# Performance work log

Hardware: AMD Instinct MI355X
Metric: run time of the kernel (lower is better)

Reference implementation:

```python
import jax, jax.numpy as jnp
import numpy as np
from jax import lax

IDC = 8          # in_dim_caps
ROUTINGS = 3
BN_EPS = 1e-5


def squash(s, axis=-1):
    mag_sq = jnp.sum(s * s, axis=axis, keepdims=True)
    mag = jnp.sqrt(mag_sq)
    return mag_sq / (1.0 + mag_sq) * (s / (mag + 1e-8))


def setup_inputs() -> dict:
    key = jax.random.key(0)
    ks = jax.random.split(key, 8)
    B, P, S = 64, 512, 8
    O, OD, Z = 32, 16, 64
    I = S * S * (P // IDC)  # 4096 input capsules
    return {
        "x": jax.random.normal(ks[0], (B, P, S, S), jnp.float32),
        "conv_w": 0.02 * jax.random.normal(ks[1], (P, P, 3, 3), jnp.float32),
        "bn_gamma": jnp.ones((P,), jnp.float32),
        "bn_beta": jnp.zeros((P,), jnp.float32),
        "bn_mean": jnp.zeros((P,), jnp.float32),
        "bn_var": jnp.ones((P,), jnp.float32),
        "caps_w": 0.01 * jax.random.normal(ks[2], (O, I, OD, IDC), jnp.float32),
        "fcm_w1": 0.02 * jax.random.normal(ks[3], (OD, 1024), jnp.float32),
        "fcm_b1": jnp.zeros((1024,), jnp.float32),
        "fcm_w2": 0.02 * jax.random.normal(ks[4], (1024, Z), jnp.float32),
        "fcm_b2": jnp.zeros((Z,), jnp.float32),
        "fcv_w": 0.02 * jax.random.normal(ks[5], (OD, Z), jnp.float32),
        "fcv_b": jnp.zeros((Z,), jnp.float32),
    }


def reference(x, conv_w, bn_gamma, bn_beta, bn_mean, bn_var, caps_w,
              fcm_w1, fcm_b1, fcm_w2, fcm_b2, fcv_w, fcv_b):
    # conv_pose: Conv3x3 (no bias) -> BatchNorm (eval, running stats) -> ReLU
    y = lax.conv_general_dilated(x, conv_w, (1, 1), 'SAME',
                                 dimension_numbers=('NCHW', 'OIHW', 'NCHW'))
    inv = bn_gamma / jnp.sqrt(bn_var + BN_EPS)
    y = (y - bn_mean[None, :, None, None]) * inv[None, :, None, None] + bn_beta[None, :, None, None]
    y = jax.nn.relu(y)

    B, P, S, _ = y.shape
    # [B, P//IDC, IDC, S, S] -> [B, P//IDC, S, S, IDC] -> [B, I, IDC]
    pose = y.reshape(B, P // IDC, IDC, S, S).transpose(0, 1, 3, 4, 2).reshape(B, -1, IDC)
    pose = squash(pose)

    # x_hat[b,o,i,d] = sum_k W[o,i,d,k] * pose[b,i,k]
    x_hat = jnp.einsum('oidk,bik->boid', caps_w, pose)
    x_hat_d = lax.stop_gradient(x_hat)

    b = jnp.zeros(x_hat.shape[:3], x_hat.dtype)  # [B, O, I]
    out = None
    for i in range(ROUTINGS):
        c = jax.nn.softmax(b, axis=1)  # softmax over output capsules
        if i == ROUTINGS - 1:
            out = squash(jnp.einsum('boi,boid->bod', c, x_hat))
        else:
            v = squash(jnp.einsum('boi,boid->bod', c, x_hat_d))
            b = b + jnp.einsum('bod,boid->boi', v, x_hat_d)

    # VAE head (eval mode: z = z_mu)
    h = jax.nn.relu(out @ fcm_w1 + fcm_b1)
    z_mu = h @ fcm_w2 + fcm_b2
    z_var = jax.nn.softplus(out @ fcv_w + fcv_b) + 1e-8
    z = z_mu
    return (z, z_mu, z_var)
```

## Files before the change

kernel.cpp:

```cpp
#include <hip/hip_runtime.h>
#include <cstdint>
#include <cstddef>

#define B 64
#define PCH 512
#define O_CAPS 32
#define OD 16
#define IDC 8
#define I_CAPS 4096
#define KDIM 4608

typedef __attribute__((ext_vector_type(8))) short bf16x8;
typedef __attribute__((ext_vector_type(4))) float f32x4;
typedef __attribute__((ext_vector_type(8))) unsigned short u16x8;
typedef _Float16 h2 __attribute__((ext_vector_type(2)));
typedef _Float16 f16x8v __attribute__((ext_vector_type(8)));

#define OFF_PH 0
#define SZ_PH (B * I_CAPS * IDC / 2)
#define OFF_PART (OFF_PH + SZ_PH)
#define SZ_PART ((size_t)256 * 4 * 16 * 512)
#define OFF_AIM OFF_PART
#define OFF_PV OFF_PART
#define OFF_CH (OFF_PART + 1048576)
#define OFF_SPILL (OFF_PART + SZ_PART)
#define OFF_VBUF (OFF_SPILL + 1048576)
#define SZ_V (B * O_CAPS * OD)
#define OFF_VBUF2 (OFF_VBUF + SZ_V)
#define OFF_OUTC (OFF_VBUF2 + SZ_V)
#define OFF_WB (OFF_OUTC + SZ_V)
#define OFF_BIAS (OFF_WB + (PCH * KDIM) / 2)
#define OFF_WRH (OFF_BIAS + 512)
#define SZ_WRH ((size_t)O_CAPS * I_CAPS * OD * IDC / 2)

__device__ inline unsigned short f2bf(float f) {
  union { float f; unsigned int u; } v; v.f = f;
  unsigned int r = v.u + 0x7fff + ((v.u >> 16) & 1);
  return (unsigned short)(r >> 16);
}

union HU { u16x8 v; f16x8v f; _Float16 h[8]; h2 p[4]; };

__device__ inline unsigned short f2h(float f) {
  union { _Float16 h; unsigned short u; } c;
  c.h = (_Float16)f;
  return c.u;
}

__device__ inline float h2f(unsigned short u) {
  union { unsigned short u; _Float16 h; } c;
  c.u = u;
  return (float)c.h;
}

__global__ __launch_bounds__(256) void cast_f16x8(
    const float* __restrict__ src, unsigned short* __restrict__ dst) {
  const size_t t = (size_t)blockIdx.x * 256 + threadIdx.x;
  const float4* s = (const float4*)src + t * 2;
  const float4 a = s[0], b = s[1];
  HU u;
  u.h[0] = (_Float16)a.x; u.h[1] = (_Float16)a.y;
  u.h[2] = (_Float16)a.z; u.h[3] = (_Float16)a.w;
  u.h[4] = (_Float16)b.x; u.h[5] = (_Float16)b.y;
  u.h[6] = (_Float16)b.z; u.h[7] = (_Float16)b.w;
  ((u16x8*)dst)[t] = u.v;
}

__global__ __launch_bounds__(256) void prep_wb(
    const float* __restrict__ cw, const float* __restrict__ gamma,
    const float* __restrict__ beta, const float* __restrict__ mean,
    const float* __restrict__ var, unsigned short* __restrict__ wb,
    float* __restrict__ bias) {
  const int n = blockIdx.x;
  const float inv = gamma[n] * rsqrtf(var[n] + 1e-5f);
  if (threadIdx.x == 0) bias[n] = beta[n] - mean[n] * inv;
  for (int k = threadIdx.x; k < KDIM; k += 256)
    wb[(size_t)n * KDIM + k] = f2bf(cw[(size_t)n * KDIM + k] * inv);
}

__global__ __launch_bounds__(256) void prep_aim(
    const float* __restrict__ x, unsigned short* __restrict__ aim) {
  __shared__ float lxp[32 * 100];
  const int b = blockIdx.x;
  const int ci0 = blockIdx.y * 32;
  const int tid = threadIdx.x;
  for (int t = tid; t < 3200; t += 256) lxp[t] = 0.f;
  __syncthreads();
  for (int t = tid; t < 2048; t += 256) {
    const int ci = t >> 6, px = t & 63;
    lxp[ci * 100 + 11 + (px >> 3) * 10 + (px & 7)] =
        x[((size_t)b * PCH + ci0 + ci) * 64 + px];
  }
  __syncthreads();
  for (int t = tid; t < 4608; t += 256) {
    const int px = t / 72;
    const int kk = (t - px * 72) * 4;
    unsigned short v[4];
#pragma unroll
    for (int j = 0; j < 4; ++j) {
      const int k = kk + j;
      const int ci = k / 9;
      const int tap = k - ci * 9;
      const int kh = tap / 3, kw = tap - kh * 3;
      v[j] = f2bf(lxp[ci * 100 + ((px >> 3) + kh) * 10 + (px & 7) + kw]);
    }
    ushort4* dst =
        (ushort4*)(aim + (size_t)(b * 64 + px) * KDIM + ci0 * 9 + kk);
    *dst = make_ushort4(v[0], v[1], v[2], v[3]);
  }
}

__global__ __launch_bounds__(256) void conv_gemm(
    const unsigned short* __restrict__ aim, const unsigned short* __restrict__ wb,
    const float* __restrict__ bias, unsigned short* __restrict__ pose_h) {
  __shared__ unsigned short lA[64 * 64];
  __shared__ unsigned short lB[64 * 64];
  const int tid = threadIdx.x;
  const int lane = tid & 63, wv = tid >> 6;
  const int wm = wv & 1, wn = wv >> 1;
  const int m0 = blockIdx.x * 64;
  const int n0 = blockIdx.y * 64;
  const int rsub = lane >> 3, seg = lane & 7;

  f32x4 acc[2][2];
#pragma unroll
  for (int a = 0; a < 2; ++a)
#pragma unroll
    for (int c = 0; c < 2; ++c) acc[a][c] = (f32x4){0.f, 0.f, 0.f, 0.f};

  for (int k0 = 0; k0 < KDIM; k0 += 64) {
    __syncthreads();
#pragma unroll
    for (int it = 0; it < 2; ++it) {
      const int r = it * 32 + wv * 8 + rsub;
      const int c = seg ^ (r & 7);
      const unsigned short* ga = aim + (size_t)(m0 + r) * KDIM + k0 + c * 8;
      __builtin_amdgcn_global_load_lds(
          (const __attribute__((address_space(1))) void*)ga,
          (__attribute__((address_space(3))) void*)(lA + (it * 32 + wv * 8) * 64),
          16, 0, 0);
      const unsigned short* gb = wb + (size_t)(n0 + r) * KDIM + k0 + c * 8;
      __builtin_amdgcn_global_load_lds(
          (const __attribute__((address_space(1))) void*)gb,
          (__attribute__((address_space(3))) void*)(lB + (it * 32 + wv * 8) * 64),
          16, 0, 0);
    }
    __syncthreads();
#pragma unroll
    for (int kc = 0; kc < 2; ++kc) {
      const int g = kc * 4 + (lane >> 4);
      const int ml = wm * 32 + (lane & 15);
      const int nl = wn * 32 + (lane & 15);
      const int sa = (g ^ (ml & 7)) * 8;
      const int sb = (g ^ (nl & 7)) * 8;
      const bf16x8 a0 = *(const bf16x8*)(lA + (ml + 0) * 64 + sa);
      const bf16x8 a1 = *(const bf16x8*)(lA + (ml + 16) * 64 + sa);
      const bf16x8 b0 = *(const bf16x8*)(lB + (nl + 0) * 64 + sb);
      const bf16x8 b1 = *(const bf16x8*)(lB + (nl + 16) * 64 + sb);
      acc[0][0] = __builtin_amdgcn_mfma_f32_16x16x32_bf16(a0, b0, acc[0][0], 0, 0, 0);
      acc[0][1] = __builtin_amdgcn_mfma_f32_16x16x32_bf16(a0, b1, acc[0][1], 0, 0, 0);
      acc[1][0] = __builtin_amdgcn_mfma_f32_16x16x32_bf16(a1, b0, acc[1][0], 0, 0, 0);
      acc[1][1] = __builtin_amdgcn_mfma_f32_16x16x32_bf16(a1, b1, acc[1][1], 0, 0, 0);
    }
  }

  const int bq = blockIdx.x;
  float bsv[2];
#pragma unroll
  for (int ni = 0; ni < 2; ++ni)
    bsv[ni] = bias[n0 + wn * 32 + ni * 16 + (lane & 15)];
#pragma unroll
  for (int mi = 0; mi < 2; ++mi) {
#pragma unroll
    for (int ni = 0; ni < 2; ++ni) {
      const int n = n0 + wn * 32 + ni * 16 + (lane & 15);
#pragma unroll
      for (int reg = 0; reg < 4; ++reg) {
        float v = fmaxf(acc[mi][ni][reg] + bsv[ni], 0.f);
        float s2 = v * v;
        s2 += __shfl_xor(s2, 1, 64);
        s2 += __shfl_xor(s2, 2, 64);
        s2 += __shfl_xor(s2, 4, 64);
        const float sc = s2 / (1.f + s2) / (sqrtf(s2) + 1e-8f);
        const int px = wm * 32 + mi * 16 + (lane >> 4) * 4 + reg;
        pose_h[((size_t)bq * I_CAPS + (n >> 3) * 64 + px) * IDC + (n & 7)] =
            f2h(v * sc);
      }
    }
  }
}

__global__ __launch_bounds__(256) void caps_v0(
    const unsigned short* __restrict__ pose_h,
    const unsigned short* __restrict__ wrh, float* __restrict__ pv) {
  __shared__ unsigned short lA[64 * 64];
  __shared__ unsigned short lB[64 * 64];
  const int tid = threadIdx.x;
  const int lane = tid & 63, wv = tid >> 6;
  const int wm = wv & 1, wn = wv >> 1;
  const int o0 = blockIdx.x * 4;
  const int ks = blockIdx.y;
  const int rsub = lane >> 3, seg = lane & 7;

  f32x4 acc[2][2];
#pragma unroll
  for (int a = 0; a < 2; ++a)
#pragma unroll
    for (int c = 0; c < 2; ++c) acc[a][c] = (f32x4){0.f, 0.f, 0.f, 0.f};

  for (int kt = 0; kt < 16; ++kt) {
    const int k0 = ks * 1024 + kt * 64;
    const int i0 = k0 >> 3;
    __syncthreads();
#pragma unroll
    for (int it = 0; it < 2; ++it) {
      const int r = it * 32 + wv * 8 + rsub;
      const int c = seg ^ (r & 7);
      const unsigned short* ga = pose_h + (size_t)r * 32768 + k0 + c * 8;
      __builtin_amdgcn_global_load_lds(
          (const __attribute__((address_space(1))) void*)ga,
          (__attribute__((address_space(3))) void*)(lA + (it * 32 + wv * 8) * 64),
          16, 0, 0);
    }
#pragma unroll
    for (int h = 0; h < 2; ++h) {
      const int idx = h * 256 + tid;
      const int d = idx & 15;
      const int il = (idx >> 4) & 7;
      const int ol = idx >> 7;
      const u16x8 v = *(const u16x8*)(wrh + (size_t)(o0 + ol) * 524288 +
                                      (size_t)(i0 + il) * 128 + d * 8);
      const int np = ol * 16 + d;
      *(u16x8*)(lB + np * 64 + (il ^ (np & 7)) * 8) = v;
    }
    __syncthreads();
#pragma unroll
    for (int kc = 0; kc < 2; ++kc) {
      const int g = kc * 4 + (lane >> 4);
      const int ml = wm * 32 + (lane & 15);
      const int nl = wn * 32 + (lane & 15);
      const int sa = (g ^ (ml & 7)) * 8;
      const int sb = (g ^ (nl & 7)) * 8;
      const f16x8v a0 = *(const f16x8v*)(lA + (ml + 0) * 64 + sa);
      const f16x8v a1 = *(const f16x8v*)(lA + (ml + 16) * 64 + sa);
      const f16x8v b0 = *(const f16x8v*)(lB + (nl + 0) * 64 + sb);
      const f16x8v b1 = *(const f16x8v*)(lB + (nl + 16) * 64 + sb);
      acc[0][0] = __builtin_amdgcn_mfma_f32_16x16x32_f16(a0, b0, acc[0][0], 0, 0, 0);
      acc[0][1] = __builtin_amdgcn_mfma_f32_16x16x32_f16(a0, b1, acc[0][1], 0, 0, 0);
      acc[1][0] = __builtin_amdgcn_mfma_f32_16x16x32_f16(a1, b0, acc[1][0], 0, 0, 0);
      acc[1][1] = __builtin_amdgcn_mfma_f32_16x16x32_f16(a1, b1, acc[1][1], 0, 0, 0);
    }
  }
#pragma unroll
  for (int mi = 0; mi < 2; ++mi) {
#pragma unroll
    for (int ni = 0; ni < 2; ++ni) {
      const int n = blockIdx.x * 64 + wn * 32 + ni * 16 + (lane & 15);
#pragma unroll
      for (int reg = 0; reg < 4; ++reg) {
        const int m = wm * 32 + mi * 16 + (lane >> 4) * 4 + reg;
        pv[(size_t)(ks * 64 + m) * 512 + n] = acc[mi][ni][reg];
      }
    }
  }
}

__global__ __launch_bounds__(256) void out_gemm(
    const unsigned short* __restrict__ pose_h,
    const unsigned short* __restrict__ wrh,
    const unsigned short* __restrict__ ch, float* __restrict__ pv) {
  __shared__ unsigned short lA[64 * 64];
  __shared__ unsigned short lB[64 * 64];
  __shared__ unsigned short clds[4 * 64 * 8];
  const int tid = threadIdx.x;
  const int lane = tid & 63, wv = tid >> 6;
  const int wm = wv & 1, wn = wv >> 1;
  const int o0 = blockIdx.x * 4;
  const int ks = blockIdx.y;
  const int rsub = lane >> 3, seg = lane & 7;
  const _Float16* chl = (const _Float16*)clds;

  f32x4 acc[2][2];
#pragma unroll
  for (int a = 0; a < 2; ++a)
#pragma unroll
    for (int c = 0; c < 2; ++c) acc[a][c] = (f32x4){0.f, 0.f, 0.f, 0.f};

  for (int kt = 0; kt < 16; ++kt) {
    const int k0 = ks * 1024 + kt * 64;
    const int i0 = k0 >> 3;
    __syncthreads();
#pragma unroll
    for (int it = 0; it < 2; ++it) {
      const int r = it * 32 + wv * 8 + rsub;
      const int c = seg ^ (r & 7);
      const unsigned short* ga = pose_h + (size_t)r * 32768 + k0 + c * 8;
      __builtin_amdgcn_global_load_lds(
          (const __attribute__((address_space(1))) void*)ga,
          (__attribute__((address_space(3))) void*)(lA + (it * 32 + wv * 8) * 64),
          16, 0, 0);
    }
#pragma unroll
    for (int h = 0; h < 2; ++h) {
      const int idx = h * 256 + tid;
      const int d = idx & 15;
      const int il = (idx >> 4) & 7;
      const int ol = idx >> 7;
      const u16x8 v = *(const u16x8*)(wrh + (size_t)(o0 + ol) * 524288 +
                                      (size_t)(i0 + il) * 128 + d * 8);
      const int np = ol * 16 + d;
      *(u16x8*)(lB + np * 64 + (il ^ (np & 7)) * 8) = v;
    }
    {
      const int o_l = tid >> 6, cb = tid & 63;
      const uint4 cv = *(const uint4*)(ch + (size_t)(o0 + o_l) * (B * I_CAPS) +
                                       (size_t)cb * I_CAPS + i0);
      *(uint4*)&clds[(o_l * 64 + cb) * 8] = cv;
    }
    __syncthreads();
#pragma unroll
    for (int kc = 0; kc < 2; ++kc) {
      const int g = kc * 4 + (lane >> 4);
      const int ml = wm * 32 + (lane & 15);
      const int nl = wn * 32 + (lane & 15);
      const int sa = (g ^ (ml & 7)) * 8;
      const int sb = (g ^ (nl & 7)) * 8;
      const f16x8v a0 = *(const f16x8v*)(lA + (ml + 0) * 64 + sa);
      const f16x8v a1 = *(const f16x8v*)(lA + (ml + 16) * 64 + sa);
      const f16x8v b0 = *(const f16x8v*)(lB + (nl + 0) * 64 + sb);
      const f16x8v b1 = *(const f16x8v*)(lB + (nl + 16) * 64 + sb);
      const int ol0 = wn * 2, ol1 = wn * 2 + 1;
      const _Float16 c00 = chl[(ol0 * 64 + ml) * 8 + g];
      const _Float16 c01 = chl[(ol1 * 64 + ml) * 8 + g];
      const _Float16 c10 = chl[(ol0 * 64 + ml + 16) * 8 + g];
      const _Float16 c11 = chl[(ol1 * 64 + ml + 16) * 8 + g];
      acc[0][0] = __builtin_amdgcn_mfma_f32_16x16x32_f16(a0 * c00, b0, acc[0][0], 0, 0, 0);
      acc[0][1] = __builtin_amdgcn_mfma_f32_16x16x32_f16(a0 * c01, b1, acc[0][1], 0, 0, 0);
      acc[1][0] = __builtin_amdgcn_mfma_f32_16x16x32_f16(a1 * c10, b0, acc[1][0], 0, 0, 0);
      acc[1][1] = __builtin_amdgcn_mfma_f32_16x16x32_f16(a1 * c11, b1, acc[1][1], 0, 0, 0);
    }
  }
#pragma unroll
  for (int mi = 0; mi < 2; ++mi) {
#pragma unroll
    for (int ni = 0; ni < 2; ++ni) {
      const int n = blockIdx.x * 64 + wn * 32 + ni * 16 + (lane & 15);
#pragma unroll
      for (int reg = 0; reg < 4; ++reg) {
        const int m = wm * 32 + mi * 16 + (lane >> 4) * 4 + reg;
        pv[(size_t)(ks * 64 + m) * 512 + n] = acc[mi][ni][reg];
      }
    }
  }
}

__global__ __launch_bounds__(256) void logits_softmax(
    const unsigned short* __restrict__ pose_h,
    const unsigned short* __restrict__ wrh,
    const float* __restrict__ vb, unsigned short* __restrict__ ch) {
  __shared__ unsigned short ppose[16 * 132];
  __shared__ float lgl[32 * 272];
  const int tid = threadIdx.x;
  const int lane = tid & 63, wv = tid >> 6;
  const int i0 = blockIdx.x * 16;
  const int b0 = blockIdx.y * 16;
  const _Float16* wh = (const _Float16*)wrh;

  {
    const int b = tid >> 4, i = tid & 15;
    const ushort4* src =
        (const ushort4*)(pose_h + ((size_t)(b0 + b) * I_CAPS + (i0 + i)) * IDC);
    const ushort4 p0 = src[0], p1 = src[1];
    *(ushort4*)&ppose[b * 132 + i * 8] = p0;
    *(ushort4*)&ppose[b * 132 + i * 8 + 4] = p1;
  }
  __syncthreads();

  const int m = lane & 15;
  const int g = lane >> 4;
  const int a_isub = m >> 3, a_kk = m & 7;
  const int c_isub = g >> 1, c_kk0 = (g & 1) * 4;

  for (int o = 0; o < 32; ++o) {
    HU bu;
    bu.v = (u16x8){0, 0, 0, 0, 0, 0, 0, 0};
    if (g < 2) {
      const float4* vp =
          (const float4*)(vb + ((size_t)(b0 + m) * O_CAPS + o) * OD + g * 8);
      const float4 v0 = vp[0], v1 = vp[1];
      bu.h[0] = (_Float16)v0.x; bu.h[1] = (_Float16)v0.y;
      bu.h[2] = (_Float16)v0.z; bu.h[3] = (_Float16)v0.w;
      bu.h[4] = (_Float16)v1.x; bu.h[5] = (_Float16)v1.y;
      bu.h[6] = (_Float16)v1.z; bu.h[7] = (_Float16)v1.w;
    }
#pragma unroll
    for (int q = 0; q < 2; ++q) {
      const int ip = wv * 2 + q;
      HU au;
      au.v = (u16x8){0, 0, 0, 0, 0, 0, 0, 0};
      if (g < 2) {
        const int ii = i0 + ip * 2 + a_isub;
        const size_t base =
            (((size_t)o * I_CAPS + ii) * OD + g * 8) * IDC + a_kk;
#pragma unroll
        for (int j = 0; j < 8; ++j) au.h[j] = wh[base + (size_t)j * IDC];
      }
      const f32x4 C = __builtin_amdgcn_mfma_f32_16x16x32_f16(
          au.f, bu.f, (f32x4){0.f, 0.f, 0.f, 0.f}, 0, 0, 0);
      const ushort4 pk =
          *(const ushort4*)&ppose[m * 132 + (ip * 2 + c_isub) * 8 + c_kk0];
      float tmp = C[0] * h2f(pk.x) + C[1] * h2f(pk.y) + C[2] * h2f(pk.z) +
                  C[3] * h2f(pk.w);
      tmp += __shfl_xor(tmp, 16, 64);
      if ((lane & 16) == 0) {
        const int iw = ip * 2 + (lane >> 5);
        lgl[o * 272 + iw * 17 + m] = tmp;
      }
    }
  }
  __syncthreads();

  {
    const int i = tid & 15, b = tid >> 4;
    float e[32];
    float sm = 0.f;
#pragma unroll
    for (int o = 0; o < 32; ++o) {
      e[o] = __expf(lgl[o * 272 + i * 17 + b]);
      sm += e[o];
    }
    const float r = 1.f / sm;
#pragma unroll
    for (int o = 0; o < 32; ++o)
      ch[(size_t)o * ((size_t)B * I_CAPS) + (size_t)(b0 + b) * I_CAPS +
         (i0 + i)] = f2h(e[o] * r);
  }
}

template <int SCALE32, int ADDV>
__global__ __launch_bounds__(256) void reduce_pv(
    const float* __restrict__ pv, const float* __restrict__ vprev,
    float* __restrict__ dst) {
  const int t = blockIdx.x * 256 + threadIdx.x;
  const int b = t >> 9;
  const int r = t & 511;
  float s = 0.f;
#pragma unroll 8
  for (int ks = 0; ks < 32; ++ks)
    s += pv[(size_t)(ks * 64 + b) * 512 + r];
  if (SCALE32) s *= (1.0f / 32.0f);
  float sq = s * s;
  sq += __shfl_xor(sq, 1, 64);
  sq += __shfl_xor(sq, 2, 64);
  sq += __shfl_xor(sq, 4, 64);
  sq += __shfl_xor(sq, 8, 64);
  const float sc = sq / (1.f + sq) / (sqrtf(sq) + 1e-8f);
  float val = s * sc;
  if (ADDV) val += vprev[t];
  dst[t] = val;
}

__global__ __launch_bounds__(1024) void vae_head(
    const float* __restrict__ outc, const float* __restrict__ w1,
    const float* __restrict__ b1, const float* __restrict__ w2,
    const float* __restrict__ b2, const float* __restrict__ wv,
    const float* __restrict__ bv, float* __restrict__ dout) {
  __shared__ float lo[4][16];
  __shared__ float lh[4][1024];
  __shared__ float red[16][4][64];
  const int n0 = blockIdx.x * 4;
  const int tid = threadIdx.x;
  if (tid < 64) lo[tid >> 4][tid & 15] = outc[(size_t)n0 * 16 + tid];
  __syncthreads();

  {
    const float bb = b1[tid];
    float h0 = bb, h1 = bb, h2v = bb, h3 = bb;
#pragma unroll
    for (int k = 0; k < 16; ++k) {
      const float w = w1[(size_t)k * 1024 + tid];
      h0 += lo[0][k] * w;
      h1 += lo[1][k] * w;
      h2v += lo[2][k] * w;
      h3 += lo[3][k] * w;
    }
    lh[0][tid] = fmaxf(h0, 0.f);
    lh[1][tid] = fmaxf(h1, 0.f);
    lh[2][tid] = fmaxf(h2v, 0.f);
    lh[3][tid] = fmaxf(h3, 0.f);
  }
  __syncthreads();

  const int m = tid & 63, sl = tid >> 6;
  {
    float a0 = 0.f, a1 = 0.f, a2 = 0.f, a3 = 0.f;
    const int j0 = sl * 64;
#pragma unroll 4
    for (int jj = 0; jj < 64; ++jj) {
      const int j = j0 + jj;
      const float w = w2[(size_t)j * 64 + m];
      a0 += lh[0][j] * w;
      a1 += lh[1][j] * w;
      a2 += lh[2][j] * w;
      a3 += lh[3][j] * w;
    }
    red[sl][0][m] = a0;
    red[sl][1][m] = a1;
    red[sl][2][m] = a2;
    red[sl][3][m] = a3;
  }
  __syncthreads();

  if (tid < 256) {
    const int r = tid >> 6;
    float z = b2[m];
#pragma unroll
    for (int s = 0; s < 16; ++s) z += red[s][r][m];
    const int n = n0 + r;
    dout[n * 64 + m] = z;
    dout[131072 + n * 64 + m] = z;
    float sv = bv[m];
#pragma unroll
    for (int k = 0; k < 16; ++k) sv += lo[r][k] * wv[(size_t)k * 64 + m];
    const float sp =
        (sv > 0.f) ? (sv + log1pf(__expf(-sv))) : log1pf(__expf(sv));
    dout[262144 + n * 64 + m] = sp + 1e-8f;
  }
}

extern "C" void kernel_launch(void* const* d_in, const int* in_sizes, int n_in,
                              void* d_out, int out_size, void* d_ws,
                              size_t ws_size, hipStream_t stream) {
  const float* x = (const float*)d_in[0];
  const float* conv_w = (const float*)d_in[1];
  const float* bn_gamma = (const float*)d_in[2];
  const float* bn_beta = (const float*)d_in[3];
  const float* bn_mean = (const float*)d_in[4];
  const float* bn_var = (const float*)d_in[5];
  const float* caps_w = (const float*)d_in[6];
  const float* fcm_w1 = (const float*)d_in[7];
  const float* fcm_b1 = (const float*)d_in[8];
  const float* fcm_w2 = (const float*)d_in[9];
  const float* fcm_b2 = (const float*)d_in[10];
  const float* fcv_w = (const float*)d_in[11];
  const float* fcv_b = (const float*)d_in[12];
  float* out = (float*)d_out;
  float* ws = (float*)d_ws;

  unsigned short* pose_h = (unsigned short*)(ws + OFF_PH);
  float* pv = ws + OFF_PV;
  unsigned short* ch = (unsigned short*)(ws + OFF_CH);
  float* vbuf = ws + OFF_VBUF;
  float* vbuf2 = ws + OFF_VBUF2;
  float* outc = ws + OFF_OUTC;
  unsigned short* wbq = (unsigned short*)(ws + OFF_WB);
  float* bias = ws + OFF_BIAS;
  unsigned short* wrh = (unsigned short*)(ws + OFF_WRH);
  unsigned short* aim = (unsigned short*)(ws + OFF_AIM);

  cast_f16x8<<<8192, 256, 0, stream>>>(caps_w, wrh);
  prep_wb<<<512, 256, 0, stream>>>(conv_w, bn_gamma, bn_beta, bn_mean, bn_var,
                                   wbq, bias);
  prep_aim<<<dim3(64, 16), 256, 0, stream>>>(x, aim);
  conv_gemm<<<dim3(64, 8), 256, 0, stream>>>(aim, wbq, bias, pose_h);

  caps_v0<<<dim3(8, 32), 256, 0, stream>>>(pose_h, wrh, pv);
  reduce_pv<1, 0><<<128, 256, 0, stream>>>(pv, nullptr, vbuf);

  logits_softmax<<<dim3(256, 4), 256, 0, stream>>>(pose_h, wrh, vbuf, ch);
  out_gemm<<<dim3(8, 32), 256, 0, stream>>>(pose_h, wrh, ch, pv);
  reduce_pv<0, 1><<<128, 256, 0, stream>>>(pv, vbuf, vbuf2);

  logits_softmax<<<dim3(256, 4), 256, 0, stream>>>(pose_h, wrh, vbuf2, ch);
  out_gemm<<<dim3(8, 32), 256, 0, stream>>>(pose_h, wrh, ch, pv);
  reduce_pv<0, 0><<<128, 256, 0, stream>>>(pv, nullptr, outc);

  vae_head<<<512, 1024, 0, stream>>>(outc, fcm_w1, fcm_b1, fcm_w2, fcm_b2,
                                     fcv_w, fcv_b, out);
}
```

Before: 380.8 us.

## Stage weight tiles through LDS and keep routing logits in registers

The logits_softmax kernel used to gather the fp16 capsule weights with strided scalar global loads inside the MFMA loop. It now loads them in chunks of 8 output capsules using coalesced 16-byte loads, transposes them into an LDS tile, and reads MFMA operands from LDS as vectors. The logits are also kept in a per-thread register array instead of a large shared buffer, which removes that LDS staging and the final sync. The costs are extra barriers per chunk, higher register pressure from the 32-element array, and a changed write pattern for ch.

```diff
diff --git a/kernel.cpp b/kernel.cpp
--- a/kernel.cpp
+++ b/kernel.cpp
@@ -9,6 +9,7 @@
 #define IDC 8
 #define I_CAPS 4096
 #define KDIM 4608
+#define OCH 8
 
 typedef __attribute__((ext_vector_type(8))) short bf16x8;
 typedef __attribute__((ext_vector_type(4))) float f32x4;
@@ -359,12 +360,11 @@
     const unsigned short* __restrict__ wrh,
     const float* __restrict__ vb, unsigned short* __restrict__ ch) {
   __shared__ unsigned short ppose[16 * 132];
-  __shared__ float lgl[32 * 272];
+  __shared__ unsigned short wlds[OCH * 16 * 8 * 16];
   const int tid = threadIdx.x;
   const int lane = tid & 63, wv = tid >> 6;
   const int i0 = blockIdx.x * 16;
   const int b0 = blockIdx.y * 16;
-  const _Float16* wh = (const _Float16*)wrh;
 
   {
     const int b = tid >> 4, i = tid & 15;
@@ -374,67 +374,86 @@
     *(ushort4*)&ppose[b * 132 + i * 8] = p0;
     *(ushort4*)&ppose[b * 132 + i * 8 + 4] = p1;
   }
-  __syncthreads();
 
   const int m = lane & 15;
   const int g = lane >> 4;
-  const int a_isub = m >> 3, a_kk = m & 7;
-  const int c_isub = g >> 1, c_kk0 = (g & 1) * 4;
-
+  const int a_kk = m & 7;
+  const int gq = g & 1;
+  const int c_isub = g >> 1;
+  const int c_kk0 = (g & 1) * 4;
+
+  const int s_o2 = tid >> 7, s_i = (tid >> 3) & 15, s_dp = tid & 7;
+  unsigned int* wl32 = (unsigned int*)wlds;
+
+  float e[32];
+
+#pragma unroll
+  for (int og = 0; og < 32; og += OCH) {
+    __syncthreads();
+#pragma unroll
+    for (int pp = 0; pp < OCH / 2; ++pp) {
+      const int ol = pp * 2 + s_o2;
+      const int o = og + ol;
+      const unsigned short* gsrc =
+          wrh + ((size_t)o * I_CAPS + (i0 + s_i)) * 128 + s_dp * 16;
+      const u16x8 wa = *(const u16x8*)gsrc;
+      const u16x8 wc = *(const u16x8*)(gsrc + 8);
+      const int rbase = (ol * 16 + s_i) * 8;
+#pragma unroll
+      for (int k = 0; k < 8; ++k) {
+        wl32[(rbase + k) * 8 + s_dp] =
+            (unsigned int)(unsigned short)wa[k] |
+            ((unsigned int)(unsigned short)wc[k] << 16);
+      }
+    }
+    __syncthreads();
+#pragma unroll
+    for (int ol = 0; ol < OCH; ++ol) {
+      const int o = og + ol;
+      HU bu;
+      bu.v = (u16x8){0, 0, 0, 0, 0, 0, 0, 0};
+      if (g < 2) {
+        const float4* vp =
+            (const float4*)(vb + ((size_t)(b0 + m) * O_CAPS + o) * OD + g * 8);
+        const float4 v0 = vp[0], v1 = vp[1];
+        bu.h[0] = (_Float16)v0.x; bu.h[1] = (_Float16)v0.y;
+        bu.h[2] = (_Float16)v0.z; bu.h[3] = (_Float16)v0.w;
+        bu.h[4] = (_Float16)v1.x; bu.h[5] = (_Float16)v1.y;
+        bu.h[6] = (_Float16)v1.z; bu.h[7] = (_Float16)v1.w;
+      }
+#pragma unroll
+      for (int q = 0; q < 2; ++q) {
+        const int ip = wv * 2 + q;
+        HU au;
+        au.v = (u16x8){0, 0, 0, 0, 0, 0, 0, 0};
+        if (g < 2) {
+          const int il = ip * 2 + (m >> 3);
+          au.v = *(const u16x8*)&wlds[((ol * 16 + il) * 8 + a_kk) * 16 + g * 8];
+        }
+        const f32x4 C = __builtin_amdgcn_mfma_f32_16x16x32_f16(
+            au.f, bu.f, (f32x4){0.f, 0.f, 0.f, 0.f}, 0, 0, 0);
+        const ushort4 pk =
+            *(const ushort4*)&ppose[m * 132 + (ip * 2 + c_isub) * 8 + c_kk0];
+        float tmp = C[0] * h2f(pk.x) + C[1] * h2f(pk.y) + C[2] * h2f(pk.z) +
+                    C[3] * h2f(pk.w);
+        tmp += __shfl_xor(tmp, 16, 64);
+        if (gq == q) e[o] = tmp;
+      }
+    }
+  }
+
+  const int iw = wv * 4 + gq * 2 + (g >> 1);
+  float sm = 0.f;
+#pragma unroll
   for (int o = 0; o < 32; ++o) {
-    HU bu;
-    bu.v = (u16x8){0, 0, 0, 0, 0, 0, 0, 0};
-    if (g < 2) {
-      const float4* vp =
-          (const float4*)(vb + ((size_t)(b0 + m) * O_CAPS + o) * OD + g * 8);
-      const float4 v0 = vp[0], v1 = vp[1];
-      bu.h[0] = (_Float16)v0.x; bu.h[1] = (_Float16)v0.y;
-      bu.h[2] = (_Float16)v0.z; bu.h[3] = (_Float16)v0.w;
-      bu.h[4] = (_Float16)v1.x; bu.h[5] = (_Float16)v1.y;
-      bu.h[6] = (_Float16)v1.z; bu.h[7] = (_Float16)v1.w;
-    }
-#pragma unroll
-    for (int q = 0; q < 2; ++q) {
-      const int ip = wv * 2 + q;
-      HU au;
-      au.v = (u16x8){0, 0, 0, 0, 0, 0, 0, 0};
-      if (g < 2) {
-        const int ii = i0 + ip * 2 + a_isub;
-        const size_t base =
-            (((size_t)o * I_CAPS + ii) * OD + g * 8) * IDC + a_kk;
-#pragma unroll
-        for (int j = 0; j < 8; ++j) au.h[j] = wh[base + (size_t)j * IDC];
-      }
-      const f32x4 C = __builtin_amdgcn_mfma_f32_16x16x32_f16(
-          au.f, bu.f, (f32x4){0.f, 0.f, 0.f, 0.f}, 0, 0, 0);
-      const ushort4 pk =
-          *(const ushort4*)&ppose[m * 132 + (ip * 2 + c_isub) * 8 + c_kk0];
-      float tmp = C[0] * h2f(pk.x) + C[1] * h2f(pk.y) + C[2] * h2f(pk.z) +
-                  C[3] * h2f(pk.w);
-      tmp += __shfl_xor(tmp, 16, 64);
-      if ((lane & 16) == 0) {
-        const int iw = ip * 2 + (lane >> 5);
-        lgl[o * 272 + iw * 17 + m] = tmp;
-      }
-    }
-  }
-  __syncthreads();
-
-  {
-    const int i = tid & 15, b = tid >> 4;
-    float e[32];
-    float sm = 0.f;
-#pragma unroll
-    for (int o = 0; o < 32; ++o) {
-      e[o] = __expf(lgl[o * 272 + i * 17 + b]);
-      sm += e[o];
-    }
-    const float r = 1.f / sm;
-#pragma unroll
-    for (int o = 0; o < 32; ++o)
-      ch[(size_t)o * ((size_t)B * I_CAPS) + (size_t)(b0 + b) * I_CAPS +
-         (i0 + i)] = f2h(e[o] * r);
-  }
+    e[o] = __expf(e[o]);
+    sm += e[o];
+  }
+  const float r = 1.f / sm;
+#pragma unroll
+  for (int o = 0; o < 32; ++o)
+    ch[(size_t)o * ((size_t)B * I_CAPS) + (size_t)(b0 + m) * I_CAPS + i0 + iw] =
+        f2h(e[o] * r);
 }
 
 template <int SCALE32, int ADDV>
```

After: 392.7 us. 3.1% more time.

## Restructure logits_softmax to compute x_hat per input capsule with vector loads

Applied to the files above, without the earlier changes.

Rewrites the routing-logit kernel so each wave handles eight input capsules and loops over all 32 output capsules in registers. The MFMA now computes x_hat[d, b] directly from a contiguous 16-byte weight row and the pose vector. The dot product with v and the softmax over output capsules are done with cross-lane shuffles, which removes the shared-memory staging, both barriers and the strided per-element half loads. Half the blocks are launched and each lane does more serial work, while three quarters of the lanes stay idle in the MFMA operand loads.

```diff
diff --git a/kernel.cpp b/kernel.cpp
--- a/kernel.cpp
+++ b/kernel.cpp
@@ -358,82 +358,45 @@
     const unsigned short* __restrict__ pose_h,
     const unsigned short* __restrict__ wrh,
     const float* __restrict__ vb, unsigned short* __restrict__ ch) {
-  __shared__ unsigned short ppose[16 * 132];
-  __shared__ float lgl[32 * 272];
   const int tid = threadIdx.x;
   const int lane = tid & 63, wv = tid >> 6;
-  const int i0 = blockIdx.x * 16;
-  const int b0 = blockIdx.y * 16;
-  const _Float16* wh = (const _Float16*)wrh;
-
-  {
-    const int b = tid >> 4, i = tid & 15;
-    const ushort4* src =
-        (const ushort4*)(pose_h + ((size_t)(b0 + b) * I_CAPS + (i0 + i)) * IDC);
-    const ushort4 p0 = src[0], p1 = src[1];
-    *(ushort4*)&ppose[b * 132 + i * 8] = p0;
-    *(ushort4*)&ppose[b * 132 + i * 8 + 4] = p1;
-  }
-  __syncthreads();
-
   const int m = lane & 15;
   const int g = lane >> 4;
-  const int a_isub = m >> 3, a_kk = m & 7;
-  const int c_isub = g >> 1, c_kk0 = (g & 1) * 4;
-
-  for (int o = 0; o < 32; ++o) {
+  const int i0 = blockIdx.x * 32 + wv * 8;
+  const int b0 = blockIdx.y * 16;
+  const bool g0 = (g == 0);
+
+  for (int ii = 0; ii < 8; ++ii) {
+    const int i = i0 + ii;
     HU bu;
     bu.v = (u16x8){0, 0, 0, 0, 0, 0, 0, 0};
-    if (g < 2) {
-      const float4* vp =
-          (const float4*)(vb + ((size_t)(b0 + m) * O_CAPS + o) * OD + g * 8);
-      const float4 v0 = vp[0], v1 = vp[1];
-      bu.h[0] = (_Float16)v0.x; bu.h[1] = (_Float16)v0.y;
-      bu.h[2] = (_Float16)v0.z; bu.h[3] = (_Float16)v0.w;
-      bu.h[4] = (_Float16)v1.x; bu.h[5] = (_Float16)v1.y;
-      bu.h[6] = (_Float16)v1.z; bu.h[7] = (_Float16)v1.w;
-    }
-#pragma unroll
-    for (int q = 0; q < 2; ++q) {
-      const int ip = wv * 2 + q;
+    if (g0)
+      bu.v = *(const u16x8*)(pose_h + ((size_t)(b0 + m) * I_CAPS + i) * IDC);
+    float e[8];
+#pragma unroll
+    for (int o = 0; o < 32; ++o) {
       HU au;
       au.v = (u16x8){0, 0, 0, 0, 0, 0, 0, 0};
-      if (g < 2) {
-        const int ii = i0 + ip * 2 + a_isub;
-        const size_t base =
-            (((size_t)o * I_CAPS + ii) * OD + g * 8) * IDC + a_kk;
-#pragma unroll
-        for (int j = 0; j < 8; ++j) au.h[j] = wh[base + (size_t)j * IDC];
-      }
+      if (g0)
+        au.v =
+            *(const u16x8*)(wrh + (((size_t)o * I_CAPS + i) * OD + m) * IDC);
       const f32x4 C = __builtin_amdgcn_mfma_f32_16x16x32_f16(
           au.f, bu.f, (f32x4){0.f, 0.f, 0.f, 0.f}, 0, 0, 0);
-      const ushort4 pk =
-          *(const ushort4*)&ppose[m * 132 + (ip * 2 + c_isub) * 8 + c_kk0];
-      float tmp = C[0] * h2f(pk.x) + C[1] * h2f(pk.y) + C[2] * h2f(pk.z) +
-                  C[3] * h2f(pk.w);
-      tmp += __shfl_xor(tmp, 16, 64);
-      if ((lane & 16) == 0) {
-        const int iw = ip * 2 + (lane >> 5);
-        lgl[o * 272 + iw * 17 + m] = tmp;
-      }
-    }
-  }
-  __syncthreads();
-
-  {
-    const int i = tid & 15, b = tid >> 4;
-    float e[32];
-    float sm = 0.f;
-#pragma unroll
-    for (int o = 0; o < 32; ++o) {
-      e[o] = __expf(lgl[o * 272 + i * 17 + b]);
-      sm += e[o];
-    }
-    const float r = 1.f / sm;
-#pragma unroll
-    for (int o = 0; o < 32; ++o)
-      ch[(size_t)o * ((size_t)B * I_CAPS) + (size_t)(b0 + b) * I_CAPS +
-         (i0 + i)] = f2h(e[o] * r);
+      const float4 v4 =
+          *(const float4*)(vb + ((size_t)(b0 + m) * O_CAPS + o) * OD + g * 4);
+      float t = C[0] * v4.x + C[1] * v4.y + C[2] * v4.z + C[3] * v4.w;
+      t += __shfl_xor(t, 16, 64);
+      t += __shfl_xor(t, 32, 64);
+      if (g == (o >> 3)) e[o & 7] = __expf(t);
+    }
+    float s = ((e[0] + e[1]) + (e[2] + e[3])) + ((e[4] + e[5]) + (e[6] + e[7]));
+    s += __shfl_xor(s, 16, 64);
+    s += __shfl_xor(s, 32, 64);
+    const float r = 1.f / s;
+#pragma unroll
+    for (int j = 0; j < 8; ++j)
+      ch[(size_t)(g * 8 + j) * ((size_t)B * I_CAPS) +
+         (size_t)(b0 + m) * I_CAPS + i] = f2h(e[j] * r);
   }
 }
 
@@ -567,11 +530,11 @@
   caps_v0<<<dim3(8, 32), 256, 0, stream>>>(pose_h, wrh, pv);
   reduce_pv<1, 0><<<128, 256, 0, stream>>>(pv, nullptr, vbuf);
 
-  logits_softmax<<<dim3(256, 4), 256, 0, stream>>>(pose_h, wrh, vbuf, ch);
+  logits_softmax<<<dim3(128, 4), 256, 0, stream>>>(pose_h, wrh, vbuf, ch);
   out_gemm<<<dim3(8, 32), 256, 0, stream>>>(pose_h, wrh, ch, pv);
   reduce_pv<0, 1><<<128, 256, 0, stream>>>(pv, vbuf, vbuf2);
 
-  logits_softmax<<<dim3(256, 4), 256, 0, stream>>>(pose_h, wrh, vbuf2, ch);
+  logits_softmax<<<dim3(128, 4), 256, 0, stream>>>(pose_h, wrh, vbuf2, ch);
   out_gemm<<<dim3(8, 32), 256, 0, stream>>>(pose_h, wrh, ch, pv);
   reduce_pv<0, 0><<<128, 256, 0, stream>>>(pv, nullptr, outc);
 
```

Measured after the change: 550.5 us. +44.5%, slower.
